# Optimization experiments

Hardware: AMD Instinct MI355X
Metric: run time of the kernel (lower is better)

The kernel has to match this reference:

```python
import jax, jax.numpy as jnp
import numpy as np

B, C, F_IN = 262144, 4, 4   # batch, num label nodes, feature dim
HID = 64                     # hidden_dim (MLP embedding dim / GCN input)
GCN_H, GCN_OUT = 32, 4
EPS = 1e-8                   # torch F.cosine_similarity eps


def _glorot(k, shape):
    lim = float(np.sqrt(6.0 / (shape[0] + shape[1])))
    return jax.random.uniform(k, shape, jnp.float32, -lim, lim)


def setup_inputs() -> dict:
    key = jax.random.key(0)
    ks = jax.random.split(key, 7)
    return dict(
        x=jax.random.normal(ks[0], (B, C, F_IN), jnp.float32),
        # LabelEmbeddingMLP: 4 -> 128 -> 64 -> HID
        W1=_glorot(ks[1], (F_IN, 128)), b1=jnp.zeros((128,), jnp.float32),
        W2=_glorot(ks[2], (128, 64)),   b2=jnp.zeros((64,), jnp.float32),
        W3=_glorot(ks[3], (64, HID)),   b3=jnp.zeros((HID,), jnp.float32),
        # GCNModel: GCNConv(HID,32) -> GCNConv(32,4)
        Wg1=_glorot(ks[4], (HID, GCN_H)), bg1=jnp.zeros((GCN_H,), jnp.float32),
        Wg2=_glorot(ks[5], (GCN_H, GCN_OUT)), bg2=jnp.zeros((GCN_OUT,), jnp.float32),
    )


def reference(x, W1, b1, W2, b2, W3, b3, Wg1, bg1, Wg2, bg2):
    # --- label embedding MLP (applied per node) ---
    h = jax.nn.relu(x @ W1 + b1)
    h = jax.nn.relu(h @ W2 + b2)
    emb = h @ W3 + b3                                    # [B, C, HID]

    # --- per-sample cosine similarity, thresholded, unioned over batch ---
    # (the torch code keeps adding edges to ONE nx.Graph across all k, so the
    #  resulting 4-node edge set is the union over the batch; edge weights are
    #  ignored because GCNConv is called without edge_weight)
    n = x / jnp.maximum(jnp.linalg.norm(x, axis=-1, keepdims=True), EPS)
    sim = jnp.einsum('bif,bjf->bij', n, n)               # [B, C, C]
    adj = (sim > 0.5).any(axis=0) & ~jnp.eye(C, dtype=bool)
    adj = adj | adj.T

    # --- GCN normalized adjacency with self-loops: D^-1/2 (A+I) D^-1/2 ---
    A = adj.astype(jnp.float32) + jnp.eye(C, dtype=jnp.float32)
    dinv = jax.lax.rsqrt(A.sum(axis=1))
    Ahat = jax.lax.stop_gradient(dinv[:, None] * A * dinv[None, :])  # graph built via .item() is detached in torch

    # --- two GCNConv layers, shared Ahat broadcast over batch ---
    g = jax.nn.relu(jnp.einsum('ij,bjh->bih', Ahat, emb @ Wg1) + bg1)  # [B, C, 32]
    out = jnp.einsum('ij,bjh->bih', Ahat, g @ Wg2) + bg2               # [B, C, 4]
    return emb, out
```

## Files before the change

kernel.cpp:

```cpp
#include <hip/hip_runtime.h>

#define NB 262144
#define NNODE (NB * 4)
#define EMB_ELEMS ((size_t)NNODE * 64)
#define ADJ_BLOCKS (NNODE / 256)

typedef __attribute__((ext_vector_type(8))) _Float16 f16x8;
typedef __attribute__((ext_vector_type(4))) float f32x4;
typedef __attribute__((ext_vector_type(4))) unsigned int u32x4;

#define OW1E  0
#define OW2T  10240
#define OW3T  27648
#define OW3GT 36864
#define OWG2A 41472
#define OF32  42752
#define IMG_BYTES 43600
#define FB2   0
#define FB3   64
#define FB3G  128
#define FBG1  160
#define FBG2  192
#define FAHAT 196

#define NWAVE 8
#define WBUF_BYTES 4096
#define SMEM_BYTES (IMG_BYTES + NWAVE * WBUF_BYTES)

__device__ __forceinline__ int kperm(int ji) {
    int kt = ji >> 5, r = ji & 31, g = r >> 3, e = r & 7;
    return kt * 32 + ((e >> 2) << 4) + (g << 2) + (e & 3);
}

template <int J>
__device__ __forceinline__ float qb(float v) {
    constexpr int ctrl = J | (J << 2) | (J << 4) | (J << 6);
    int r = __builtin_amdgcn_update_dpp(0, __builtin_bit_cast(int, v), ctrl, 0xF, 0xF, true);
    return __builtin_bit_cast(float, r);
}

__global__ __launch_bounds__(256) void adj_kernel(const float* __restrict__ x,
                                                  unsigned int* __restrict__ mask_arr) {
    __shared__ unsigned int smask;
    if (threadIdx.x == 0) smask = 0u;
    __syncthreads();

    const int t = blockIdx.x * 256 + threadIdx.x;
    const int c = t & 3;
    f32x4 v = *(const f32x4*)(x + (size_t)t * 4);
    float nn = sqrtf(v.x * v.x + v.y * v.y + v.z * v.z + v.w * v.w);
    float inv = 1.0f / fmaxf(nn, 1e-8f);

    unsigned int m = 0u;
#define DOTJ(J) do {                                                            \
        const float bx = qb<J>(v.x), by = qb<J>(v.y);                           \
        const float bz = qb<J>(v.z), bw = qb<J>(v.w);                           \
        const float bi = qb<J>(inv);                                            \
        const float d = v.x * bx + v.y * by + v.z * bz + v.w * bw;              \
        if ((int)((J) != c) & (int)(d * inv * bi > 0.5f)) {                     \
            const int i_ = c < (J) ? c : (J);                                   \
            const int j_ = c < (J) ? (J) : c;                                   \
            m |= 1u << (2 * i_ + j_ - 1 - (i_ >> 1));                           \
        }                                                                       \
    } while (0)
    DOTJ(0); DOTJ(1); DOTJ(2); DOTJ(3);
#undef DOTJ

    unsigned wm = 0u;
#pragma unroll
    for (int p = 0; p < 6; ++p)
        if (__ballot((m >> p) & 1u)) wm |= (1u << p);
    if ((threadIdx.x & 63) == 0 && wm) atomicOr(&smask, wm);
    __syncthreads();
    if (threadIdx.x == 0) mask_arr[blockIdx.x] = smask;
}

__global__ __launch_bounds__(256) void prep_kernel(
    const float* __restrict__ W1, const float* __restrict__ b1,
    const float* __restrict__ W2, const float* __restrict__ b2,
    const float* __restrict__ W3, const float* __restrict__ b3,
    const float* __restrict__ Wg1, const float* __restrict__ bg1,
    const float* __restrict__ Wg2, const float* __restrict__ bg2,
    const unsigned int* __restrict__ mask_arr, char* __restrict__ img)
{
    const int t = threadIdx.x;
    const int bid = blockIdx.x;
    _Float16* H = (_Float16*)img;
    float* F = (float*)(img + OF32);

    if (bid == 0) {
        __shared__ unsigned red[256];
        unsigned um = 0u;
        for (int i = t; i < ADJ_BLOCKS; i += 256) um |= mask_arr[i];
        red[t] = um;
        __syncthreads();
        for (int s = 128; s > 0; s >>= 1) {
            if (t < s) red[t] |= red[t + s];
            __syncthreads();
        }
        const unsigned m = red[0];

        for (int i = t; i < 64; i += 256) F[FB2 + i] = b2[i];
        for (int i = t; i < 64; i += 256) F[FB3 + i] = b3[i];
        for (int i = t; i < 32; i += 256) {
            float s = 0.f;
            for (int h = 0; h < 64; ++h) s = fmaf(b3[h], Wg1[h * 32 + i], s);
            F[FB3G + i] = s;
        }
        for (int i = t; i < 32; i += 256) F[FBG1 + i] = bg1[i];
        for (int i = t; i < 4; i += 256) F[FBG2 + i] = bg2[i];
        for (int i = t; i < 16 * 40; i += 256) {
            int o = i / 40, ji = i % 40;
            float v = (o < 4 && ji < 32) ? Wg2[kperm(ji) * 4 + o] : 0.f;
            H[OWG2A / 2 + i] = (_Float16)v;
        }
        if (t == 0) {
            float A[4][4];
            for (int i = 0; i < 4; ++i)
                for (int j = 0; j < 4; ++j) A[i][j] = (i == j) ? 1.f : 0.f;
            int bit = 0;
            for (int i = 0; i < 4; ++i)
                for (int j = i + 1; j < 4; ++j) {
                    if ((m >> bit) & 1u) { A[i][j] = 1.f; A[j][i] = 1.f; }
                    ++bit;
                }
            float dinv[4];
            for (int i = 0; i < 4; ++i)
                dinv[i] = 1.0f / sqrtf(A[i][0] + A[i][1] + A[i][2] + A[i][3]);
            for (int i = 0; i < 4; ++i)
                for (int j = 0; j < 4; ++j) F[FAHAT + i * 4 + j] = dinv[i] * A[i][j] * dinv[j];
        }
    } else if (bid == 1) {
        for (int i = t; i < 128 * 40; i += 256) {
            int j = i / 40, kk = i % 40;
            float v = (kk < 4) ? W1[kk * 128 + j] : (kk == 4 ? b1[j] : 0.f);
            H[OW1E / 2 + i] = (_Float16)v;
        }
    } else if (bid == 2) {
        for (int i = t; i < 64 * 136; i += 256) {
            int jo = i / 136, ji = i % 136;
            float v = 0.f;
            if (ji < 128) v = W2[kperm(ji) * 64 + jo];
            H[OW2T / 2 + i] = (_Float16)v;
        }
    } else {
        for (int i = t; i < 64 * 72; i += 256) {
            int h = i / 72, j = i % 72;
            float v = 0.f;
            if (j < 64) v = W3[kperm(j) * 64 + h];
            H[OW3T / 2 + i] = (_Float16)v;
        }
        for (int i = t; i < 32 * 72; i += 256) {
            int e = i / 72, j = i % 72;
            float s = 0.f;
            if (j < 64) {
                const int jj = kperm(j);
                for (int h = 0; h < 64; ++h) s = fmaf(W3[jj * 64 + h], Wg1[h * 32 + e], s);
            }
            H[OW3GT / 2 + i] = (_Float16)s;
        }
    }
}

__device__ __forceinline__ unsigned pkf16(float a, float b) {
    unsigned short ha = __builtin_bit_cast(unsigned short, (_Float16)a);
    unsigned short hb = __builtin_bit_cast(unsigned short, (_Float16)b);
    return (unsigned)ha | ((unsigned)hb << 16);
}
__device__ __forceinline__ f32x4 MF(f16x8 a, f16x8 b, f32x4 c) {
    return __builtin_amdgcn_mfma_f32_16x16x32_f16(a, b, c, 0, 0, 0);
}
__device__ __forceinline__ f16x8 ldA(const _Float16* p) {
    return *(const f16x8*)p;
}
__device__ __forceinline__ f16x8 bcat(unsigned X0, unsigned X1,
                                      unsigned Y0, unsigned Y1) {
    u32x4 t; t.x = X0; t.y = X1; t.z = Y0; t.w = Y1;
    return __builtin_bit_cast(f16x8, t);
}

__global__ __launch_bounds__(512, 4) void mlp_gcn_mfma(
    const float* __restrict__ x, const char* __restrict__ img,
    float* __restrict__ emb_out, float* __restrict__ out_out)
{
    __shared__ u32x4 smem4[SMEM_BYTES / 16];
    char* smem = (char*)smem4;
    const int tx = threadIdx.x;
    {
        const u32x4* src = (const u32x4*)img;
        u32x4* dst = (u32x4*)smem;
        for (int i = tx; i < IMG_BYTES / 16; i += 512) dst[i] = src[i];
    }
    __syncthreads();

    const _Float16* wh = (const _Float16*)smem;
    const float* wf = (const float*)(smem + OF32);

    const int wid = tx >> 6, lane = tx & 63;
    const int g = lane >> 4, c = lane & 15;
    const bool g0 = (g == 0);

    float* tb = (float*)(smem + IMG_BYTES) + wid * 1024;

    const size_t nbase0 = ((size_t)blockIdx.x * NWAVE + wid) * 256;

#pragma unroll 1
    for (int it = 0; it < 4; ++it) {
        const size_t nbase = nbase0 + (size_t)it * 64;

        f16x8 xB[4];
#pragma unroll
        for (int nt = 0; nt < 4; ++nt) {
            f32x4 xq = *(const f32x4*)(x + (nbase + nt * 16 + c) * 4);
            u32x4 t;
            t.x = g0 ? pkf16(xq.x, xq.y) : 0u;
            t.y = g0 ? pkf16(xq.z, xq.w) : 0u;
            t.z = g0 ? 0x00003C00u : 0u;
            t.w = 0u;
            xB[nt] = __builtin_bit_cast(f16x8, t);
        }

        f32x4 acc2[4][4];
#pragma unroll
        for (int mt = 0; mt < 4; ++mt) {
            f32x4 bv = *(const f32x4*)(wf + FB2 + mt * 16 + g * 4);
#pragma unroll
            for (int nt = 0; nt < 4; ++nt) acc2[mt][nt] = bv;
        }
#pragma unroll
        for (int kt = 0; kt < 4; ++kt) {
            f16x8 a0 = ldA(wh + OW1E / 2 + ((2 * kt + 0) * 16 + c) * 40 + g * 8);
            f16x8 a1 = ldA(wh + OW1E / 2 + ((2 * kt + 1) * 16 + c) * 40 + g * 8);
            f16x8 bf[4];
#pragma unroll
            for (int nt = 0; nt < 4; ++nt) {
                f32x4 z = {0.f, 0.f, 0.f, 0.f};
                f32x4 t0 = MF(a0, xB[nt], z);
                f32x4 t1 = MF(a1, xB[nt], z);
                bf[nt] = bcat(pkf16(fmaxf(t0[0], 0.f), fmaxf(t0[1], 0.f)),
                              pkf16(fmaxf(t0[2], 0.f), fmaxf(t0[3], 0.f)),
                              pkf16(fmaxf(t1[0], 0.f), fmaxf(t1[1], 0.f)),
                              pkf16(fmaxf(t1[2], 0.f), fmaxf(t1[3], 0.f)));
            }
#pragma unroll
            for (int mt = 0; mt < 4; ++mt) {
                f16x8 a = ldA(wh + OW2T / 2 + (mt * 16 + c) * 136 + kt * 32 + g * 8);
#pragma unroll
                for (int nt = 0; nt < 4; ++nt) acc2[mt][nt] = MF(a, bf[nt], acc2[mt][nt]);
            }
        }

        unsigned pk2a[4][4][2];
#pragma unroll
        for (int mt = 0; mt < 4; ++mt)
#pragma unroll
            for (int nt = 0; nt < 4; ++nt) {
                pk2a[mt][nt][0] = pkf16(fmaxf(acc2[mt][nt][0], 0.f), fmaxf(acc2[mt][nt][1], 0.f));
                pk2a[mt][nt][1] = pkf16(fmaxf(acc2[mt][nt][2], 0.f), fmaxf(acc2[mt][nt][3], 0.f));
            }

        {
            f32x4 acc4[2][4];
#pragma unroll
            for (int mt = 0; mt < 2; ++mt) {
                f32x4 bv = *(const f32x4*)(wf + FB3G + mt * 16 + g * 4);
#pragma unroll
                for (int nt = 0; nt < 4; ++nt) acc4[mt][nt] = bv;
            }
#pragma unroll
            for (int kt = 0; kt < 2; ++kt) {
#pragma unroll
                for (int mt = 0; mt < 2; ++mt) {
                    f16x8 a = ldA(wh + OW3GT / 2 + (mt * 16 + c) * 72 + kt * 32 + g * 8);
#pragma unroll
                    for (int nt = 0; nt < 4; ++nt) {
                        f16x8 bf = bcat(pk2a[2 * kt][nt][0], pk2a[2 * kt][nt][1],
                                        pk2a[2 * kt + 1][nt][0], pk2a[2 * kt + 1][nt][1]);
                        acc4[mt][nt] = MF(a, bf, acc4[mt][nt]);
                    }
                }
            }
            const f32x4 arow = *(const f32x4*)(wf + FAHAT + (c & 3) * 4);
            f32x4 bg1v[2];
            bg1v[0] = *(const f32x4*)(wf + FBG1 + g * 4);
            bg1v[1] = *(const f32x4*)(wf + FBG1 + 16 + g * 4);
            const f32x4 bg2v = *(const f32x4*)(wf + FBG2);
            const f16x8 aWg2 = ldA(wh + OWG2A / 2 + c * 40 + g * 8);
#pragma unroll
            for (int nt = 0; nt < 4; ++nt) {
                float gv[2][4];
#pragma unroll
                for (int m = 0; m < 2; ++m)
#pragma unroll
                    for (int r = 0; r < 4; ++r) {
                        float v = acc4[m][nt][r];
                        float s = bg1v[m][r];
                        s = fmaf(arow.x, qb<0>(v), s);
                        s = fmaf(arow.y, qb<1>(v), s);
                        s = fmaf(arow.z, qb<2>(v), s);
                        s = fmaf(arow.w, qb<3>(v), s);
                        gv[m][r] = fmaxf(s, 0.f);
                    }
                f16x8 bfg = bcat(pkf16(gv[0][0], gv[0][1]), pkf16(gv[0][2], gv[0][3]),
                                 pkf16(gv[1][0], gv[1][1]), pkf16(gv[1][2], gv[1][3]));
                f32x4 z = {0.f, 0.f, 0.f, 0.f};
                f32x4 u4 = MF(aWg2, bfg, z);
                float ov[4];
#pragma unroll
                for (int o = 0; o < 4; ++o) {
                    float s = bg2v[o];
                    s = fmaf(arow.x, qb<0>(u4[o]), s);
                    s = fmaf(arow.y, qb<1>(u4[o]), s);
                    s = fmaf(arow.z, qb<2>(u4[o]), s);
                    s = fmaf(arow.w, qb<3>(u4[o]), s);
                    ov[o] = s;
                }
                if (g0) {
                    f32x4 t; t.x = ov[0]; t.y = ov[1]; t.z = ov[2]; t.w = ov[3];
                    *(f32x4*)(out_out + (nbase + nt * 16 + c) * 4) = t;
                }
            }
        }

#pragma unroll 1
        for (int mh = 0; mh < 2; ++mh) {
            f32x4 acc3h[2][4];
#pragma unroll
            for (int mt2 = 0; mt2 < 2; ++mt2) {
                f32x4 bv = *(const f32x4*)(wf + FB3 + (mh * 2 + mt2) * 16 + g * 4);
#pragma unroll
                for (int nt = 0; nt < 4; ++nt) acc3h[mt2][nt] = bv;
            }
#pragma unroll
            for (int kt = 0; kt < 2; ++kt) {
#pragma unroll
                for (int mt2 = 0; mt2 < 2; ++mt2) {
                    const int mt = mh * 2 + mt2;
                    f16x8 a = ldA(wh + OW3T / 2 + (mt * 16 + c) * 72 + kt * 32 + g * 8);
#pragma unroll
                    for (int nt = 0; nt < 4; ++nt) {
                        f16x8 bf = bcat(pk2a[2 * kt][nt][0], pk2a[2 * kt][nt][1],
                                        pk2a[2 * kt + 1][nt][0], pk2a[2 * kt + 1][nt][1]);
                        acc3h[mt2][nt] = MF(a, bf, acc3h[mt2][nt]);
                    }
                }
            }
#pragma unroll
            for (int nt = 0; nt < 4; ++nt) {
#pragma unroll
                for (int mt2 = 0; mt2 < 2; ++mt2) {
                    int sl = (mt2 * 4 + g) ^ (c & 7);
                    *(f32x4*)(tb + c * 36 + sl * 4) = acc3h[mt2][nt];
                }
                float* gp = emb_out + (nbase + nt * 16) * 64 + mh * 32;
#pragma unroll
                for (int s = 0; s < 2; ++s) {
                    int F = s * 64 + lane;
                    int node = F >> 3, col4 = F & 7;
                    int sl = col4 ^ (node & 7);
                    f32x4 q = *(const f32x4*)(tb + node * 36 + sl * 4);
                    *(f32x4*)(gp + node * 64 + col4 * 4) = q;
                }
            }
        }
    }
}

extern "C" void kernel_launch(void* const* d_in, const int* in_sizes, int n_in,
                              void* d_out, int out_size, void* d_ws, size_t ws_size,
                              hipStream_t stream) {
    const float* x   = (const float*)d_in[0];
    const float* W1  = (const float*)d_in[1];
    const float* b1  = (const float*)d_in[2];
    const float* W2  = (const float*)d_in[3];
    const float* b2  = (const float*)d_in[4];
    const float* W3  = (const float*)d_in[5];
    const float* b3  = (const float*)d_in[6];
    const float* Wg1 = (const float*)d_in[7];
    const float* bg1 = (const float*)d_in[8];
    const float* Wg2 = (const float*)d_in[9];
    const float* bg2 = (const float*)d_in[10];

    unsigned int* mask_arr = (unsigned int*)d_ws;
    char* img = (char*)d_ws + 16640;

    float* emb_out = (float*)d_out;
    float* out_out = emb_out + EMB_ELEMS;

    adj_kernel<<<ADJ_BLOCKS, 256, 0, stream>>>(x, mask_arr);
    prep_kernel<<<4, 256, 0, stream>>>(W1, b1, W2, b2, W3, b3, Wg1, bg1, Wg2, bg2,
                                       mask_arr, img);
    mlp_gcn_mfma<<<NNODE / 2048, 512, 0, stream>>>(x, img, emb_out, out_out);
}
```

Before: 111.0 us.

## Fuse adjacency, weight prep and MLP-GCN into one cooperative kernel

Replaces the three-kernel chain (adjacency mask, weight-image prep, main MFMA kernel) with one cooperative kernel of 512 blocks. Each block computes adjacency bits for its own slice of x, publishes them, and waits at a grid-wide sync. Every block then reduces the masks, builds Ahat and the fp16 weight image directly in shared memory, and runs the main body. This removes two kernel launches and the global image round-trip. In exchange, every block redundantly rebuilds the weight image (including a 64-term W3·Wg1 product) and pays for a grid barrier. It falls back to the old path if the cooperative launch fails.

Result: slower. 314.3 us (+183.1%).

```diff
diff --git a/kernel.cpp b/kernel.cpp
--- a/kernel.cpp
+++ b/kernel.cpp
@@ -1,4 +1,7 @@
 #include <hip/hip_runtime.h>
+#include <hip/hip_cooperative_groups.h>
+
+namespace cg = cooperative_groups;
 
 #define NB 262144
 #define NNODE (NB * 4)
@@ -39,19 +42,27 @@
     return __builtin_bit_cast(float, r);
 }
 
-__global__ __launch_bounds__(256) void adj_kernel(const float* __restrict__ x,
-                                                  unsigned int* __restrict__ mask_arr) {
-    __shared__ unsigned int smask;
-    if (threadIdx.x == 0) smask = 0u;
-    __syncthreads();
-
-    const int t = blockIdx.x * 256 + threadIdx.x;
-    const int c = t & 3;
-    f32x4 v = *(const f32x4*)(x + (size_t)t * 4);
+__device__ __forceinline__ unsigned pkf16(float a, float b) {
+    unsigned short ha = __builtin_bit_cast(unsigned short, (_Float16)a);
+    unsigned short hb = __builtin_bit_cast(unsigned short, (_Float16)b);
+    return (unsigned)ha | ((unsigned)hb << 16);
+}
+__device__ __forceinline__ f32x4 MF(f16x8 a, f16x8 b, f32x4 c) {
+    return __builtin_amdgcn_mfma_f32_16x16x32_f16(a, b, c, 0, 0, 0);
+}
+__device__ __forceinline__ f16x8 ldA(const _Float16* p) {
+    return *(const f16x8*)p;
+}
+__device__ __forceinline__ f16x8 bcat(unsigned X0, unsigned X1,
+                                      unsigned Y0, unsigned Y1) {
+    u32x4 t; t.x = X0; t.y = X1; t.z = Y0; t.w = Y1;
+    return __builtin_bit_cast(f16x8, t);
+}
+
+__device__ __forceinline__ unsigned adj_bits(f32x4 v, int c) {
     float nn = sqrtf(v.x * v.x + v.y * v.y + v.z * v.z + v.w * v.w);
     float inv = 1.0f / fmaxf(nn, 1e-8f);
-
-    unsigned int m = 0u;
+    unsigned m = 0u;
 #define DOTJ(J) do {                                                            \
         const float bx = qb<J>(v.x), by = qb<J>(v.y);                           \
         const float bz = qb<J>(v.z), bw = qb<J>(v.w);                           \
@@ -65,144 +76,85 @@
     } while (0)
     DOTJ(0); DOTJ(1); DOTJ(2); DOTJ(3);
 #undef DOTJ
-
-    unsigned wm = 0u;
-#pragma unroll
-    for (int p = 0; p < 6; ++p)
-        if (__ballot((m >> p) & 1u)) wm |= (1u << p);
-    if ((threadIdx.x & 63) == 0 && wm) atomicOr(&smask, wm);
-    __syncthreads();
-    if (threadIdx.x == 0) mask_arr[blockIdx.x] = smask;
-}
-
-__global__ __launch_bounds__(256) void prep_kernel(
+    return m;
+}
+
+template <int NT>
+__device__ void build_image(int t,
     const float* __restrict__ W1, const float* __restrict__ b1,
     const float* __restrict__ W2, const float* __restrict__ b2,
     const float* __restrict__ W3, const float* __restrict__ b3,
     const float* __restrict__ Wg1, const float* __restrict__ bg1,
     const float* __restrict__ Wg2, const float* __restrict__ bg2,
-    const unsigned int* __restrict__ mask_arr, char* __restrict__ img)
+    _Float16* H, float* F)
 {
-    const int t = threadIdx.x;
-    const int bid = blockIdx.x;
-    _Float16* H = (_Float16*)img;
-    float* F = (float*)(img + OF32);
-
-    if (bid == 0) {
-        __shared__ unsigned red[256];
-        unsigned um = 0u;
-        for (int i = t; i < ADJ_BLOCKS; i += 256) um |= mask_arr[i];
-        red[t] = um;
-        __syncthreads();
-        for (int s = 128; s > 0; s >>= 1) {
-            if (t < s) red[t] |= red[t + s];
-            __syncthreads();
-        }
-        const unsigned m = red[0];
-
-        for (int i = t; i < 64; i += 256) F[FB2 + i] = b2[i];
-        for (int i = t; i < 64; i += 256) F[FB3 + i] = b3[i];
-        for (int i = t; i < 32; i += 256) {
-            float s = 0.f;
-            for (int h = 0; h < 64; ++h) s = fmaf(b3[h], Wg1[h * 32 + i], s);
-            F[FB3G + i] = s;
-        }
-        for (int i = t; i < 32; i += 256) F[FBG1 + i] = bg1[i];
-        for (int i = t; i < 4; i += 256) F[FBG2 + i] = bg2[i];
-        for (int i = t; i < 16 * 40; i += 256) {
-            int o = i / 40, ji = i % 40;
-            float v = (o < 4 && ji < 32) ? Wg2[kperm(ji) * 4 + o] : 0.f;
-            H[OWG2A / 2 + i] = (_Float16)v;
-        }
-        if (t == 0) {
-            float A[4][4];
-            for (int i = 0; i < 4; ++i)
-                for (int j = 0; j < 4; ++j) A[i][j] = (i == j) ? 1.f : 0.f;
-            int bit = 0;
-            for (int i = 0; i < 4; ++i)
-                for (int j = i + 1; j < 4; ++j) {
-                    if ((m >> bit) & 1u) { A[i][j] = 1.f; A[j][i] = 1.f; }
-                    ++bit;
-                }
-            float dinv[4];
-            for (int i = 0; i < 4; ++i)
-                dinv[i] = 1.0f / sqrtf(A[i][0] + A[i][1] + A[i][2] + A[i][3]);
-            for (int i = 0; i < 4; ++i)
-                for (int j = 0; j < 4; ++j) F[FAHAT + i * 4 + j] = dinv[i] * A[i][j] * dinv[j];
-        }
-    } else if (bid == 1) {
-        for (int i = t; i < 128 * 40; i += 256) {
-            int j = i / 40, kk = i % 40;
-            float v = (kk < 4) ? W1[kk * 128 + j] : (kk == 4 ? b1[j] : 0.f);
-            H[OW1E / 2 + i] = (_Float16)v;
-        }
-    } else if (bid == 2) {
-        for (int i = t; i < 64 * 136; i += 256) {
-            int jo = i / 136, ji = i % 136;
-            float v = 0.f;
-            if (ji < 128) v = W2[kperm(ji) * 64 + jo];
-            H[OW2T / 2 + i] = (_Float16)v;
-        }
-    } else {
-        for (int i = t; i < 64 * 72; i += 256) {
-            int h = i / 72, j = i % 72;
-            float v = 0.f;
-            if (j < 64) v = W3[kperm(j) * 64 + h];
-            H[OW3T / 2 + i] = (_Float16)v;
-        }
-        for (int i = t; i < 32 * 72; i += 256) {
-            int e = i / 72, j = i % 72;
-            float s = 0.f;
-            if (j < 64) {
-                const int jj = kperm(j);
-                for (int h = 0; h < 64; ++h) s = fmaf(W3[jj * 64 + h], Wg1[h * 32 + e], s);
-            }
-            H[OW3GT / 2 + i] = (_Float16)s;
-        }
-    }
-}
-
-__device__ __forceinline__ unsigned pkf16(float a, float b) {
-    unsigned short ha = __builtin_bit_cast(unsigned short, (_Float16)a);
-    unsigned short hb = __builtin_bit_cast(unsigned short, (_Float16)b);
-    return (unsigned)ha | ((unsigned)hb << 16);
-}
-__device__ __forceinline__ f32x4 MF(f16x8 a, f16x8 b, f32x4 c) {
-    return __builtin_amdgcn_mfma_f32_16x16x32_f16(a, b, c, 0, 0, 0);
-}
-__device__ __forceinline__ f16x8 ldA(const _Float16* p) {
-    return *(const f16x8*)p;
-}
-__device__ __forceinline__ f16x8 bcat(unsigned X0, unsigned X1,
-                                      unsigned Y0, unsigned Y1) {
-    u32x4 t; t.x = X0; t.y = X1; t.z = Y0; t.w = Y1;
-    return __builtin_bit_cast(f16x8, t);
-}
-
-__global__ __launch_bounds__(512, 4) void mlp_gcn_mfma(
-    const float* __restrict__ x, const char* __restrict__ img,
-    float* __restrict__ emb_out, float* __restrict__ out_out)
+    for (int i = t; i < 128 * 40; i += NT) {
+        int j = i / 40, kk = i % 40;
+        float v = (kk < 4) ? W1[kk * 128 + j] : (kk == 4 ? b1[j] : 0.f);
+        H[OW1E / 2 + i] = (_Float16)v;
+    }
+    for (int i = t; i < 64 * 136; i += NT) {
+        int jo = i / 136, ji = i % 136;
+        float v = 0.f;
+        if (ji < 128) v = W2[kperm(ji) * 64 + jo];
+        H[OW2T / 2 + i] = (_Float16)v;
+    }
+    for (int i = t; i < 64 * 72; i += NT) {
+        int h = i / 72, j = i % 72;
+        float v = 0.f;
+        if (j < 64) v = W3[kperm(j) * 64 + h];
+        H[OW3T / 2 + i] = (_Float16)v;
+    }
+    for (int i = t; i < 32 * 72; i += NT) {
+        int e = i / 72, j = i % 72;
+        float s = 0.f;
+        if (j < 64) {
+            const int jj = kperm(j);
+            for (int h = 0; h < 64; ++h) s = fmaf(W3[jj * 64 + h], Wg1[h * 32 + e], s);
+        }
+        H[OW3GT / 2 + i] = (_Float16)s;
+    }
+    for (int i = t; i < 16 * 40; i += NT) {
+        int o = i / 40, ji = i % 40;
+        float v = (o < 4 && ji < 32) ? Wg2[kperm(ji) * 4 + o] : 0.f;
+        H[OWG2A / 2 + i] = (_Float16)v;
+    }
+    for (int i = t; i < 64; i += NT) F[FB2 + i] = b2[i];
+    for (int i = t; i < 64; i += NT) F[FB3 + i] = b3[i];
+    for (int i = t; i < 32; i += NT) {
+        float s = 0.f;
+        for (int h = 0; h < 64; ++h) s = fmaf(b3[h], Wg1[h * 32 + i], s);
+        F[FB3G + i] = s;
+    }
+    for (int i = t; i < 32; i += NT) F[FBG1 + i] = bg1[i];
+    for (int i = t; i < 4; i += NT) F[FBG2 + i] = bg2[i];
+}
+
+__device__ __forceinline__ void build_ahat(unsigned m, float* F) {
+    float A[4][4];
+    for (int i = 0; i < 4; ++i)
+        for (int j = 0; j < 4; ++j) A[i][j] = (i == j) ? 1.f : 0.f;
+    int bit = 0;
+    for (int i = 0; i < 4; ++i)
+        for (int j = i + 1; j < 4; ++j) {
+            if ((m >> bit) & 1u) { A[i][j] = 1.f; A[j][i] = 1.f; }
+            ++bit;
+        }
+    float dinv[4];
+    for (int i = 0; i < 4; ++i)
+        dinv[i] = 1.0f / sqrtf(A[i][0] + A[i][1] + A[i][2] + A[i][3]);
+    for (int i = 0; i < 4; ++i)
+        for (int j = 0; j < 4; ++j) F[FAHAT + i * 4 + j] = dinv[i] * A[i][j] * dinv[j];
+}
+
+__device__ void main_body(const float* __restrict__ x,
+                          const _Float16* wh, const float* wf, float* tb,
+                          int tx, float* __restrict__ emb_out,
+                          float* __restrict__ out_out, size_t nbase0)
 {
-    __shared__ u32x4 smem4[SMEM_BYTES / 16];
-    char* smem = (char*)smem4;
-    const int tx = threadIdx.x;
-    {
-        const u32x4* src = (const u32x4*)img;
-        u32x4* dst = (u32x4*)smem;
-        for (int i = tx; i < IMG_BYTES / 16; i += 512) dst[i] = src[i];
-    }
-    __syncthreads();
-
-    const _Float16* wh = (const _Float16*)smem;
-    const float* wf = (const float*)(smem + OF32);
-
-    const int wid = tx >> 6, lane = tx & 63;
+    const int lane = tx & 63;
     const int g = lane >> 4, c = lane & 15;
     const bool g0 = (g == 0);
-
-    float* tb = (float*)(smem + IMG_BYTES) + wid * 1024;
-
-    const size_t nbase0 = ((size_t)blockIdx.x * NWAVE + wid) * 256;
 
 #pragma unroll 1
     for (int it = 0; it < 4; ++it) {
@@ -366,6 +318,135 @@
     }
 }
 
+__global__ __launch_bounds__(512, 4) void fused_kernel(
+    const float* __restrict__ x,
+    const float* __restrict__ W1, const float* __restrict__ b1,
+    const float* __restrict__ W2, const float* __restrict__ b2,
+    const float* __restrict__ W3, const float* __restrict__ b3,
+    const float* __restrict__ Wg1, const float* __restrict__ bg1,
+    const float* __restrict__ Wg2, const float* __restrict__ bg2,
+    unsigned int* __restrict__ ws,
+    float* __restrict__ emb_out, float* __restrict__ out_out)
+{
+    __shared__ u32x4 smem4[SMEM_BYTES / 16];
+    char* smem = (char*)smem4;
+    _Float16* H = (_Float16*)smem;
+    float* F = (float*)(smem + OF32);
+    unsigned* wsc = (unsigned*)(smem + IMG_BYTES);
+    const int tx = threadIdx.x;
+    const int wid = tx >> 6;
+    const size_t nbase0 = ((size_t)blockIdx.x * NWAVE + wid) * 256;
+
+    unsigned m = 0u;
+#pragma unroll 1
+    for (int sc = 0; sc < 4; ++sc) {
+        const int t = blockIdx.x * 2048 + sc * 512 + tx;
+        const int c = t & 3;
+        f32x4 v = *(const f32x4*)(x + (size_t)t * 4);
+        m |= adj_bits(v, c);
+    }
+    unsigned wm = 0u;
+#pragma unroll
+    for (int p = 0; p < 6; ++p)
+        if (__ballot((m >> p) & 1u)) wm |= (1u << p);
+    if ((tx & 63) == 0) wsc[wid] = wm;
+    __syncthreads();
+    if (tx == 0) {
+        unsigned bm = 0u;
+        for (int w = 0; w < NWAVE; ++w) bm |= wsc[w];
+        __hip_atomic_store(&ws[blockIdx.x], bm, __ATOMIC_RELEASE,
+                           __HIP_MEMORY_SCOPE_AGENT);
+    }
+    cg::this_grid().sync();
+
+    {
+        unsigned um = __hip_atomic_load(&ws[tx], __ATOMIC_ACQUIRE,
+                                        __HIP_MEMORY_SCOPE_AGENT);
+        unsigned wm2 = 0u;
+#pragma unroll
+        for (int p = 0; p < 6; ++p)
+            if (__ballot((um >> p) & 1u)) wm2 |= (1u << p);
+        __syncthreads();
+        if ((tx & 63) == 0) wsc[wid] = wm2;
+        __syncthreads();
+        if (tx == 0) {
+            unsigned gm = 0u;
+            for (int w = 0; w < NWAVE; ++w) gm |= wsc[w];
+            build_ahat(gm, F);
+        }
+        build_image<512>(tx, W1, b1, W2, b2, W3, b3, Wg1, bg1, Wg2, bg2, H, F);
+        __syncthreads();
+    }
+
+    float* tb = (float*)(smem + IMG_BYTES) + wid * 1024;
+    main_body(x, (const _Float16*)smem, (const float*)(smem + OF32), tb,
+              tx, emb_out, out_out, nbase0);
+}
+
+__global__ __launch_bounds__(256) void adj_kernel(const float* __restrict__ x,
+                                                  unsigned int* __restrict__ mask_arr) {
+    __shared__ unsigned int smask;
+    if (threadIdx.x == 0) smask = 0u;
+    __syncthreads();
+    const int t = blockIdx.x * 256 + threadIdx.x;
+    f32x4 v = *(const f32x4*)(x + (size_t)t * 4);
+    unsigned m = adj_bits(v, t & 3);
+    unsigned wm = 0u;
+#pragma unroll
+    for (int p = 0; p < 6; ++p)
+        if (__ballot((m >> p) & 1u)) wm |= (1u << p);
+    if ((threadIdx.x & 63) == 0 && wm) atomicOr(&smask, wm);
+    __syncthreads();
+    if (threadIdx.x == 0) mask_arr[blockIdx.x] = smask;
+}
+
+__global__ __launch_bounds__(256) void prep_kernel(
+    const float* __restrict__ W1, const float* __restrict__ b1,
+    const float* __restrict__ W2, const float* __restrict__ b2,
+    const float* __restrict__ W3, const float* __restrict__ b3,
+    const float* __restrict__ Wg1, const float* __restrict__ bg1,
+    const float* __restrict__ Wg2, const float* __restrict__ bg2,
+    const unsigned int* __restrict__ mask_arr, char* __restrict__ img)
+{
+    const int t = threadIdx.x;
+    _Float16* H = (_Float16*)img;
+    float* F = (float*)(img + OF32);
+    if (blockIdx.x == 0) {
+        __shared__ unsigned red[256];
+        unsigned um = 0u;
+        for (int i = t; i < ADJ_BLOCKS; i += 256) um |= mask_arr[i];
+        red[t] = um;
+        __syncthreads();
+        for (int s = 128; s > 0; s >>= 1) {
+            if (t < s) red[t] |= red[t + s];
+            __syncthreads();
+        }
+        if (t == 0) build_ahat(red[0], F);
+    } else if (blockIdx.x == 1) {
+        build_image<256>(t, W1, b1, W2, b2, W3, b3, Wg1, bg1, Wg2, bg2, H, F);
+    }
+}
+
+__global__ __launch_bounds__(512, 4) void mlp_gcn_mfma(
+    const float* __restrict__ x, const char* __restrict__ img,
+    float* __restrict__ emb_out, float* __restrict__ out_out)
+{
+    __shared__ u32x4 smem4[SMEM_BYTES / 16];
+    char* smem = (char*)smem4;
+    const int tx = threadIdx.x;
+    {
+        const u32x4* src = (const u32x4*)img;
+        u32x4* dst = (u32x4*)smem;
+        for (int i = tx; i < IMG_BYTES / 16; i += 512) dst[i] = src[i];
+    }
+    __syncthreads();
+    const int wid = tx >> 6;
+    float* tb = (float*)(smem + IMG_BYTES) + wid * 1024;
+    const size_t nbase0 = ((size_t)blockIdx.x * NWAVE + wid) * 256;
+    main_body(x, (const _Float16*)smem, (const float*)(smem + OF32), tb,
+              tx, emb_out, out_out, nbase0);
+}
+
 extern "C" void kernel_launch(void* const* d_in, const int* in_sizes, int n_in,
                               void* d_out, int out_size, void* d_ws, size_t ws_size,
                               hipStream_t stream) {
@@ -381,14 +462,23 @@
     const float* Wg2 = (const float*)d_in[9];
     const float* bg2 = (const float*)d_in[10];
 
-    unsigned int* mask_arr = (unsigned int*)d_ws;
+    unsigned int* ws_masks = (unsigned int*)d_ws;
     char* img = (char*)d_ws + 16640;
 
     float* emb_out = (float*)d_out;
     float* out_out = emb_out + EMB_ELEMS;
 
-    adj_kernel<<<ADJ_BLOCKS, 256, 0, stream>>>(x, mask_arr);
-    prep_kernel<<<4, 256, 0, stream>>>(W1, b1, W2, b2, W3, b3, Wg1, bg1, Wg2, bg2,
-                                       mask_arr, img);
-    mlp_gcn_mfma<<<NNODE / 2048, 512, 0, stream>>>(x, img, emb_out, out_out);
-}
+    void* args[] = { (void*)&x, (void*)&W1, (void*)&b1, (void*)&W2, (void*)&b2,
+                     (void*)&W3, (void*)&b3, (void*)&Wg1, (void*)&bg1,
+                     (void*)&Wg2, (void*)&bg2, (void*)&ws_masks,
+                     (void*)&emb_out, (void*)&out_out };
+    hipError_t err = hipLaunchCooperativeKernel((void*)fused_kernel,
+                                                dim3(512), dim3(512), args, 0, stream);
+    if (err != hipSuccess) {
+        (void)hipGetLastError();
+        adj_kernel<<<ADJ_BLOCKS, 256, 0, stream>>>(x, ws_masks);
+        prep_kernel<<<2, 256, 0, stream>>>(W1, b1, W2, b2, W3, b3, Wg1, bg1,
+                                           Wg2, bg2, ws_masks, img);
+        mlp_gcn_mfma<<<NNODE / 2048, 512, 0, stream>>>(x, img, emb_out, out_out);
+    }
+}
```
